# Kernel optimization log

Hardware: AMD Instinct MI355X
Metric: run time of the kernel (lower is better)

The kernel has to match this reference:

```python
import jax, jax.numpy as jnp
import numpy as np

RADIUS = 0.5
BATCH, N, C_IN, C_OUT = 8, 1024, 64, 64


def setup_inputs() -> dict:
    key = jax.random.key(0)
    k1, k2, k3 = jax.random.split(key, 3)
    features = jax.random.normal(k1, (BATCH, N, C_IN), dtype=jnp.float32)
    geometry = jax.random.normal(k2, (BATCH, N, 3), dtype=jnp.float32)
    # Kernel stand-in: linear map from relative position to [C_out, C_in] matrix
    W = jax.random.normal(k3, (3, C_OUT, C_IN), dtype=jnp.float32) / np.sqrt(3.0 * C_IN)
    return {"features": features, "geometry": geometry, "W": W}


def reference(features, geometry, W):
    # diff[z,a,b,:] = r_b - r_a  (neighbor minus center), matching rb - ra in torch
    diff = geometry[:, None, :, :] - geometry[:, :, None, :]          # [z,a,b,3]
    norm = jnp.sqrt(jnp.sum(diff * diff, axis=-1))                    # [z,a,b]
    # rel_mask: 1 where within radius (the dense equivalent of the padded
    # neighbor-list + mask; padded/out-of-ball entries contribute zero)
    rel_mask = (norm < RADIUS).astype(features.dtype)                 # [z,a,b]
    # kernel(diff)[z,a,b,i,j] = sum_x diff[z,a,b,x] * W[x,i,j]
    # output[z,a,i] = sum_{b,x,j} mask*diff[z,a,b,x] * W[x,i,j] * feat[z,b,j]
    mdiff = rel_mask[..., None] * diff                                # [z,a,b,3]
    tmp = jnp.einsum('zabx,zbj->zaxj', mdiff, features)               # [z,a,3,Cin]
    out = jnp.einsum('zaxj,xij->zai', tmp, W)                         # [z,a,Cout]
    return out
```

## Files before the change

### kernel.cpp

```cpp
#include <hip/hip_runtime.h>


#define BATCHSZ 8
#define NPTS 1024
#define CIN 64
#define COUT 64
#define NXJ (3 * CIN)
#define NG (NXJ / 4)
#define PPB 8
#define BS (PPB * 64)
#define CAP 128
#define GPW (NG / PPB)

typedef float f32x2 __attribute__((ext_vector_type(2)));

#define SM_LR 3072
#define SM_TMP 7168
#define SM_TOTAL 8704

__global__ __launch_bounds__(256) void transpose_W_kernel(
    const float* __restrict__ W,
    float* __restrict__ Wt)
{
    const int t = blockIdx.x * 256 + threadIdx.x;
    if (t >= 3 * COUT * CIN) return;
    const int x = t >> 12;
    const int i = (t >> 6) & 63;
    const int j = t & 63;
    const int xj = x * CIN + j;
    Wt[((xj >> 2) * COUT + i) * 4 + (xj & 3)] = W[t];
}

template <bool WT>
__global__ __launch_bounds__(BS, 4) void neigh_conv_kernel(
    const float* __restrict__ feat,
    const float* __restrict__ geom,
    const float* __restrict__ Wv,
    float* __restrict__ out)
{
    const int lane = threadIdx.x & 63;
    const int wv   = threadIdx.x >> 6;
    const int p    = blockIdx.x * PPB + wv;
    const int a    = p & (NPTS - 1);
    const int z    = p >> 10;

    __shared__ __align__(16) float smem[SM_TOTAL];

    {
        const float4* src = (const float4*)(geom + (size_t)z * NPTS * 3);
        float4* dst = (float4*)smem;
        for (int k = threadIdx.x; k < NPTS * 3 / 4; k += BS)
            dst[k] = src[k];
    }
    __syncthreads();

    const float* geo = smem;
    const float gax = geo[a * 3 + 0];
    const float gay = geo[a * 3 + 1];
    const float gaz = geo[a * 3 + 2];
    const float* fz = feat + (size_t)z * NPTS * CIN;

    float4* list4 = (float4*)(smem + SM_LR) + wv * CAP;
    const unsigned long long ltmask = (1ull << lane) - 1ull;

    f32x2 axy = {0.f, 0.f};
    float az2 = 0.f;
    int nn = 0;

    const float4* g4 = (const float4*)geo;
    for (int ss = 0; ss < 4; ++ss) {
        const int fbase = ss * 192 + lane * 3;
        const float4 q0 = g4[fbase + 0];
        const float4 q1 = g4[fbase + 1];
        const float4 q2 = g4[fbase + 2];
        float cx[4] = {q0.x, q0.w, q1.z, q2.y};
        float cy[4] = {q0.y, q1.x, q1.w, q2.z};
        float cz[4] = {q0.z, q1.y, q2.x, q2.w};
        #pragma unroll
        for (int s = 0; s < 4; ++s) {
            float dx, dy, dz, d2;
            {
                #pragma clang fp contract(off)
                dx = cx[s] - gax;
                dy = cy[s] - gay;
                dz = cz[s] - gaz;
                d2 = dx * dx + dy * dy + dz * dz;
            }
            const bool hit = d2 < 0.25f;
            const unsigned long long m = __ballot(hit);
            const int c = __popcll(m);
            const int b = ss * 256 + 4 * lane + s;
            if (nn + c <= CAP) {
                if (hit) {
                    const int slot = nn + __popcll(m & ltmask);
                    float4 e;
                    e.x = dx; e.y = dy; e.z = dz; e.w = __int_as_float(b);
                    list4[slot] = e;
                }
                nn += c;
            } else {
                unsigned long long mm = m;
                while (mm) {
                    const int src = __ffsll(mm) - 1;
                    mm &= mm - 1ull;
                    const float ddx = __shfl(dx, src);
                    const float ddy = __shfl(dy, src);
                    const float ddz = __shfl(dz, src);
                    const int bsrc = ss * 256 + 4 * src + s;
                    const float f = fz[(size_t)bsrc * CIN + lane];
                    axy.x = fmaf(ddx, f, axy.x);
                    axy.y = fmaf(ddy, f, axy.y);
                    az2   = fmaf(ddz, f, az2);
                }
            }
        }
    }

    {
        const int npad = (4 - (nn & 3)) & 3;
        if (lane < npad) {
            float4 e;
            e.x = 0.f; e.y = 0.f; e.z = 0.f; e.w = __int_as_float(a);
            list4[nn + lane] = e;
        }
        nn += npad;
    }

    for (int k = 0; k < nn; k += 4) {
        const float4 e0 = list4[k + 0];
        const float4 e1 = list4[k + 1];
        const float4 e2 = list4[k + 2];
        const float4 e3 = list4[k + 3];
        const float f0 = fz[(size_t)__float_as_int(e0.w) * CIN + lane];
        const float f1 = fz[(size_t)__float_as_int(e1.w) * CIN + lane];
        const float f2 = fz[(size_t)__float_as_int(e2.w) * CIN + lane];
        const float f3 = fz[(size_t)__float_as_int(e3.w) * CIN + lane];
        f32x2 d01; d01.x = e0.x; d01.y = e0.y;
        f32x2 d11; d11.x = e1.x; d11.y = e1.y;
        f32x2 d21; d21.x = e2.x; d21.y = e2.y;
        f32x2 d31; d31.x = e3.x; d31.y = e3.y;
        f32x2 ff0 = {f0, f0}, ff1 = {f1, f1}, ff2 = {f2, f2}, ff3 = {f3, f3};
        axy = d01 * ff0 + axy;  az2 = fmaf(e0.z, f0, az2);
        axy = d11 * ff1 + axy;  az2 = fmaf(e1.z, f1, az2);
        axy = d21 * ff2 + axy;  az2 = fmaf(e2.z, f2, az2);
        axy = d31 * ff3 + axy;  az2 = fmaf(e3.z, f3, az2);
    }

    float* tmp = smem + SM_TMP + wv * NXJ;
    tmp[0 * CIN + lane] = axy.x;
    tmp[1 * CIN + lane] = axy.y;
    tmp[2 * CIN + lane] = az2;
    __syncthreads();

    const int g0 = wv * GPW;
    float4 wr[GPW];
    if (WT) {
        const float4* w4 = (const float4*)Wv;
        #pragma unroll
        for (int q = 0; q < GPW; ++q)
            wr[q] = w4[(g0 + q) * COUT + lane];
    } else {
        #pragma unroll
        for (int q = 0; q < GPW; ++q) {
            const int xj = 4 * (g0 + q);
            wr[q].x = Wv[((xj + 0) >> 6) * 4096 + lane * 64 + ((xj + 0) & 63)];
            wr[q].y = Wv[((xj + 1) >> 6) * 4096 + lane * 64 + ((xj + 1) & 63)];
            wr[q].z = Wv[((xj + 2) >> 6) * 4096 + lane * 64 + ((xj + 2) & 63)];
            wr[q].w = Wv[((xj + 3) >> 6) * 4096 + lane * 64 + ((xj + 3) & 63)];
        }
    }

    float* red = smem + SM_LR;
    #pragma unroll
    for (int pp = 0; pp < PPB; ++pp) {
        const float4* t4 = (const float4*)(smem + SM_TMP + pp * NXJ);
        f32x2 facc = {0.f, 0.f};
        #pragma unroll
        for (int q = 0; q < GPW; ++q) {
            const float4 t = t4[g0 + q];
            f32x2 ta; ta.x = t.x; ta.y = t.y;
            f32x2 tb; tb.x = t.z; tb.y = t.w;
            f32x2 wa; wa.x = wr[q].x; wa.y = wr[q].y;
            f32x2 wb; wb.x = wr[q].z; wb.y = wr[q].w;
            facc = ta * wa + facc;
            facc = tb * wb + facc;
        }
        red[(wv * PPB + pp) * COUT + lane] = facc.x + facc.y;
    }
    __syncthreads();

    float o = 0.f;
    #pragma unroll
    for (int w = 0; w < PPB; ++w)
        o += red[(w * PPB + wv) * COUT + lane];

    out[(size_t)p * COUT + lane] = o;
}

extern "C" void kernel_launch(void* const* d_in, const int* in_sizes, int n_in,
                              void* d_out, int out_size, void* d_ws, size_t ws_size,
                              hipStream_t stream) {
    const float* feat = (const float*)d_in[0];
    const float* geom = (const float*)d_in[1];
    const float* W    = (const float*)d_in[2];
    float* out        = (float*)d_out;

    const int nblocks = BATCHSZ * NPTS / PPB;

    if (ws_size >= (size_t)(3 * COUT * CIN) * sizeof(float)) {
        float* Wt = (float*)d_ws;
        transpose_W_kernel<<<(3 * COUT * CIN + 255) / 256, 256, 0, stream>>>(W, Wt);
        neigh_conv_kernel<true><<<nblocks, BS, 0, stream>>>(feat, geom, Wt, out);
    } else {
        neigh_conv_kernel<false><<<nblocks, BS, 0, stream>>>(feat, geom, W, out);
    }
}
```

Baseline: 22.29 us.

## Drop shared geometry staging and cross-wave W split; per-wave full contraction

Each wave now reads geometry straight from global memory instead of the block staging the whole batch's coordinates into LDS. Blocks shrink from 8 to 4 waves, and the neighbor list capacity drops from 128 to 64. Each wave now runs the full 192-wide contraction against W on its own instead of splitting W across waves and reducing through LDS. This removes the block-wide barriers and the cross-wave reduction, but each wave reloads all of W from cache and does strided, uncoalesced geometry loads. The smaller capacity also sends more neighbors down the slower shuffle-based overflow path.

```diff
diff --git a/kernel.cpp b/kernel.cpp
--- a/kernel.cpp
+++ b/kernel.cpp
@@ -5,18 +5,12 @@
 #define NPTS 1024
 #define CIN 64
 #define COUT 64
-#define NXJ (3 * CIN)
-#define NG (NXJ / 4)
-#define PPB 8
-#define BS (PPB * 64)
-#define CAP 128
-#define GPW (NG / PPB)
+#define NG 48
+#define WPB 4
+#define BS (WPB * 64)
+#define CAP 64
 
 typedef float f32x2 __attribute__((ext_vector_type(2)));
-
-#define SM_LR 3072
-#define SM_TMP 7168
-#define SM_TOTAL 8704
 
 __global__ __launch_bounds__(256) void transpose_W_kernel(
     const float* __restrict__ W,
@@ -32,7 +26,7 @@
 }
 
 template <bool WT>
-__global__ __launch_bounds__(BS, 4) void neigh_conv_kernel(
+__global__ __launch_bounds__(BS, 8) void neigh_conv_kernel(
     const float* __restrict__ feat,
     const float* __restrict__ geom,
     const float* __restrict__ Wv,
@@ -40,78 +34,61 @@
 {
     const int lane = threadIdx.x & 63;
     const int wv   = threadIdx.x >> 6;
-    const int p    = blockIdx.x * PPB + wv;
+    const int p    = blockIdx.x * WPB + wv;
     const int a    = p & (NPTS - 1);
     const int z    = p >> 10;
 
-    __shared__ __align__(16) float smem[SM_TOTAL];
+    __shared__ __align__(16) float4 list[WPB][CAP];
+    __shared__ __align__(16) float  tmp[WPB][3 * CIN];
 
-    {
-        const float4* src = (const float4*)(geom + (size_t)z * NPTS * 3);
-        float4* dst = (float4*)smem;
-        for (int k = threadIdx.x; k < NPTS * 3 / 4; k += BS)
-            dst[k] = src[k];
-    }
-    __syncthreads();
+    const float* gz = geom + (size_t)z * NPTS * 3;
+    const float* fz = feat + (size_t)z * NPTS * CIN;
+    const float gax = gz[a * 3 + 0];
+    const float gay = gz[a * 3 + 1];
+    const float gaz = gz[a * 3 + 2];
 
-    const float* geo = smem;
-    const float gax = geo[a * 3 + 0];
-    const float gay = geo[a * 3 + 1];
-    const float gaz = geo[a * 3 + 2];
-    const float* fz = feat + (size_t)z * NPTS * CIN;
-
-    float4* list4 = (float4*)(smem + SM_LR) + wv * CAP;
+    float4* list4 = list[wv];
     const unsigned long long ltmask = (1ull << lane) - 1ull;
 
     f32x2 axy = {0.f, 0.f};
     float az2 = 0.f;
     int nn = 0;
 
-    const float4* g4 = (const float4*)geo;
-    for (int ss = 0; ss < 4; ++ss) {
-        const int fbase = ss * 192 + lane * 3;
-        const float4 q0 = g4[fbase + 0];
-        const float4 q1 = g4[fbase + 1];
-        const float4 q2 = g4[fbase + 2];
-        float cx[4] = {q0.x, q0.w, q1.z, q2.y};
-        float cy[4] = {q0.y, q1.x, q1.w, q2.z};
-        float cz[4] = {q0.z, q1.y, q2.x, q2.w};
-        #pragma unroll
-        for (int s = 0; s < 4; ++s) {
-            float dx, dy, dz, d2;
-            {
-                #pragma clang fp contract(off)
-                dx = cx[s] - gax;
-                dy = cy[s] - gay;
-                dz = cz[s] - gaz;
-                d2 = dx * dx + dy * dy + dz * dz;
+    #pragma unroll 4
+    for (int bb = 0; bb < NPTS; bb += 64) {
+        const int b = bb + lane;
+        const float* gp = gz + (size_t)b * 3;
+        float dx, dy, dz, d2;
+        {
+            #pragma clang fp contract(off)
+            dx = gp[0] - gax;
+            dy = gp[1] - gay;
+            dz = gp[2] - gaz;
+            d2 = dx * dx + dy * dy + dz * dz;
+        }
+        const bool hit = d2 < 0.25f;
+        const unsigned long long m = __ballot(hit);
+        const int c = __popcll(m);
+        if (nn + c <= CAP) {
+            if (hit) {
+                const int slot = nn + __popcll(m & ltmask);
+                float4 e;
+                e.x = dx; e.y = dy; e.z = dz; e.w = __int_as_float(b);
+                list4[slot] = e;
             }
-            const bool hit = d2 < 0.25f;
-            const unsigned long long m = __ballot(hit);
-            const int c = __popcll(m);
-            const int b = ss * 256 + 4 * lane + s;
-            if (nn + c <= CAP) {
-                if (hit) {
-                    const int slot = nn + __popcll(m & ltmask);
-                    float4 e;
-                    e.x = dx; e.y = dy; e.z = dz; e.w = __int_as_float(b);
-                    list4[slot] = e;
-                }
-                nn += c;
-            } else {
-                unsigned long long mm = m;
-                while (mm) {
-                    const int src = __ffsll(mm) - 1;
-                    mm &= mm - 1ull;
-                    const float ddx = __shfl(dx, src);
-                    const float ddy = __shfl(dy, src);
-                    const float ddz = __shfl(dz, src);
-                    const int bsrc = ss * 256 + 4 * src + s;
-                    const float f = fz[(size_t)bsrc * CIN + lane];
-                    axy.x = fmaf(ddx, f, axy.x);
-                    axy.y = fmaf(ddy, f, axy.y);
-                    az2   = fmaf(ddz, f, az2);
-                }
+            nn += c;
+        } else {
+            unsigned long long mm = m;
+            while (mm) {
+                const int src = __ffsll(mm) - 1;
+                mm &= mm - 1ull;
+                const float ddx = __shfl(dx, src);
+                const float ddy = __shfl(dy, src);
+                const float ddz = __shfl(dz, src);
+                const float f = fz[(size_t)(bb + src) * CIN + lane];
+                axy.x = fmaf(ddx, f, axy.x);
+                axy.y = fmaf(ddy, f, axy.y);
+                az2   = fmaf(ddz, f, az2);
             }
         }
     }
@@ -135,66 +112,54 @@
         const float f1 = fz[(size_t)__float_as_int(e1.w) * CIN + lane];
         const float f2 = fz[(size_t)__float_as_int(e2.w) * CIN + lane];
         const float f3 = fz[(size_t)__float_as_int(e3.w) * CIN + lane];
-        f32x2 d01; d01.x = e0.x; d01.y = e0.y;
-        f32x2 d11; d11.x = e1.x; d11.y = e1.y;
-        f32x2 d21; d21.x = e2.x; d21.y = e2.y;
-        f32x2 d31; d31.x = e3.x; d31.y = e3.y;
+        f32x2 d0; d0.x = e0.x; d0.y = e0.y;
+        f32x2 d1; d1.x = e1.x; d1.y = e1.y;
+        f32x2 d2; d2.x = e2.x; d2.y = e2.y;
+        f32x2 d3; d3.x = e3.x; d3.y = e3.y;
         f32x2 ff0 = {f0, f0}, ff1 = {f1, f1}, ff2 = {f2, f2}, ff3 = {f3, f3};
-        axy = d01 * ff0 + axy;  az2 = fmaf(e0.z, f0, az2);
-        axy = d11 * ff1 + axy;  az2 = fmaf(e1.z, f1, az2);
-        axy = d21 * ff2 + axy;  az2 = fmaf(e2.z, f2, az2);
-        axy = d31 * ff3 + axy;  az2 = fmaf(e3.z, f3, az2);
+        axy = d0 * ff0 + axy;  az2 = fmaf(e0.z, f0, az2);
+        axy = d1 * ff1 + axy;  az2 = fmaf(e1.z, f1, az2);
+        axy = d2 * ff2 + axy;  az2 = fmaf(e2.z, f2, az2);
+        axy = d3 * ff3 + axy;  az2 = fmaf(e3.z, f3, az2);
     }
 
-    float* tmp = smem + SM_TMP + wv * NXJ;
-    tmp[0 * CIN + lane] = axy.x;
-    tmp[1 * CIN + lane] = axy.y;
-    tmp[2 * CIN + lane] = az2;
-    __syncthreads();
+    float* tw = tmp[wv];
+    tw[0 * CIN + lane] = axy.x;
+    tw[1 * CIN + lane] = axy.y;
+    tw[2 * CIN + lane] = az2;
 
-    const int g0 = wv * GPW;
-    float4 wr[GPW];
+    const float4* t4 = (const float4*)tw;
+    f32x2 facc = {0.f, 0.f};
     if (WT) {
         const float4* w4 = (const float4*)Wv;
-        #pragma unroll
-        for (int q = 0; q < GPW; ++q)
-            wr[q] = w4[(g0 + q) * COUT + lane];
+        #pragma unroll 4
+        for (int g = 0; g < NG; ++g) {
+            const float4 t = t4[g];
+            const float4 w = w4[g * COUT + lane];
+            f32x2 ta; ta.x = t.x; ta.y = t.y;
+            f32x2 tb; tb.x = t.z; tb.y = t.w;
+            f32x2 wa; wa.x = w.x; wa.y = w.y;
+            f32x2 wb; wb.x = w.z; wb.y = w.w;
+            facc = ta * wa + facc;
+            facc = tb * wb + facc;
+        }
     } else {
-        #pragma unroll
-        for (int q = 0; q < GPW; ++q) {
-            const int xj = 4 * (g0 + q);
-            wr[q].x = Wv[((xj + 0) >> 6) * 4096 + lane * 64 + ((xj + 0) & 63)];
-            wr[q].y = Wv[((xj + 1) >> 6) * 4096 + lane * 64 + ((xj + 1) & 63)];
-            wr[q].z = Wv[((xj + 2) >> 6) * 4096 + lane * 64 + ((xj + 2) & 63)];
-            wr[q].w = Wv[((xj + 3) >> 6) * 4096 + lane * 64 + ((xj + 3) & 63)];
+        #pragma unroll 4
+        for (int g = 0; g < NG; ++g) {
+            const float4 t = t4[g];
+            const int xj = 4 * g;
+            float w0 = Wv[((xj + 0) >> 6) * 4096 + lane * 64 + ((xj + 0) & 63)];
+            float w1 = Wv[((xj + 1) >> 6) * 4096 + lane * 64 + ((xj + 1) & 63)];
+            float w2 = Wv[((xj + 2) >> 6) * 4096 + lane * 64 + ((xj + 2) & 63)];
+            float w3 = Wv[((xj + 3) >> 6) * 4096 + lane * 64 + ((xj + 3) & 63)];
+            facc.x = fmaf(t.x, w0, facc.x);
+            facc.y = fmaf(t.y, w1, facc.y);
+            facc.x = fmaf(t.z, w2, facc.x);
+            facc.y = fmaf(t.w, w3, facc.y);
         }
     }
 
-    float* red = smem + SM_LR;
-    #pragma unroll
-    for (int pp = 0; pp < PPB; ++pp) {
-        const float4* t4 = (const float4*)(smem + SM_TMP + pp * NXJ);
-        f32x2 facc = {0.f, 0.f};
-        #pragma unroll
-        for (int q = 0; q < GPW; ++q) {
-            const float4 t = t4[g0 + q];
-            f32x2 ta; ta.x = t.x; ta.y = t.y;
-            f32x2 tb; tb.x = t.z; tb.y = t.w;
-            f32x2 wa; wa.x = wr[q].x; wa.y = wr[q].y;
-            f32x2 wb; wb.x = wr[q].z; wb.y = wr[q].w;
-            facc = ta * wa + facc;
-            facc = tb * wb + facc;
-        }
-        red[(wv * PPB + pp) * COUT + lane] = facc.x + facc.y;
-    }
-    __syncthreads();
-
-    float o = 0.f;
-    #pragma unroll
-    for (int w = 0; w < PPB; ++w)
-        o += red[(w * PPB + wv) * COUT + lane];
-
-    out[(size_t)p * COUT + lane] = o;
+    out[(size_t)p * COUT + lane] = facc.x + facc.y;
 }
 
 extern "C" void kernel_launch(void* const* d_in, const int* in_sizes, int n_in,
@@ -205,7 +170,7 @@
     const float* W    = (const float*)d_in[2];
     float* out        = (float*)d_out;
 
-    const int nblocks = BATCHSZ * NPTS / PPB;
+    const int nblocks = BATCHSZ * NPTS / WPB;
 
     if (ws_size >= (size_t)(3 * COUT * CIN) * sizeof(float)) {
         float* Wt = (float*)d_ws;
```

Result: slower. 27.59 us (+23.8%).
